# Kernel optimization log

Measured on AMD Instinct MI355X. Metric: run time of the kernel, lower is better.

Reference implementation:

```python
import jax, jax.numpy as jnp
import numpy as np

B, T, I, H, L, O = 2048, 512, 1, 64, 2, 1


def _lstm_layer(x, Wih, Whh, b):
    """Single LSTM layer, batch_first x: [B, T, in] -> [B, T, H].
    PyTorch gate order: i, f, g, o. b = b_ih + b_hh (folded)."""
    Bn = x.shape[0]
    Hn = Whh.shape[1]
    # Precompute input contribution for all timesteps (hoisted out of scan)
    xg = jnp.einsum('bti,gi->btg', x, Wih) + b  # [B, T, 4H]

    def step(carry, xg_t):
        h, c = carry
        g = xg_t + h @ Whh.T  # [B, 4H]
        i, f, gg, o = jnp.split(g, 4, axis=-1)
        i = jax.nn.sigmoid(i)
        f = jax.nn.sigmoid(f)
        gg = jnp.tanh(gg)
        o = jax.nn.sigmoid(o)
        c = f * c + i * gg
        h = o * jnp.tanh(c)
        return (h, c), h

    h0 = jnp.zeros((Bn, Hn), x.dtype)
    c0 = jnp.zeros((Bn, Hn), x.dtype)
    (_, _), hs = jax.lax.scan(step, (h0, c0), jnp.swapaxes(xg, 0, 1))  # hs: [T, B, H]
    return jnp.swapaxes(hs, 0, 1)


def setup_inputs() -> dict:
    key = jax.random.key(0)
    ks = jax.random.split(key, 11)
    s = 1.0 / np.sqrt(H)  # torch default uniform bound
    u = lambda k, shp: jax.random.uniform(k, shp, jnp.float32, -s, s)
    return {
        'x': jax.random.normal(ks[0], (B, T, I), jnp.float32),
        'Wih0': u(ks[1], (4 * H, I)),
        'Whh0': u(ks[2], (4 * H, H)),
        'bih0': u(ks[3], (4 * H,)),
        'bhh0': u(ks[4], (4 * H,)),
        'Wih1': u(ks[5], (4 * H, H)),
        'Whh1': u(ks[6], (4 * H, H)),
        'bih1': u(ks[7], (4 * H,)),
        'bhh1': u(ks[8], (4 * H,)),
        'fcW': u(ks[9], (O, H)),
        'fcb': u(ks[10], (O,)),
    }


def reference(x, Wih0, Whh0, bih0, bhh0, Wih1, Whh1, bih1, bhh1, fcW, fcb):
    h1 = _lstm_layer(x, Wih0, Whh0, bih0 + bhh0)   # [B, T, H]
    h2 = _lstm_layer(h1, Wih1, Whh1, bih1 + bhh1)  # [B, T, H]
    return h2[:, -1, :] @ fcW.T + fcb               # [B, O]
```

## Files before the change

### kernel.cpp

```cpp
#include <hip/hip_runtime.h>


#define TT 512
#define HH 64
#define BT 8

typedef __attribute__((ext_vector_type(4))) int i32x4;

#define MFMAI8 __builtin_amdgcn_mfma_i32_16x16x64_i8

#define WSCALE 260096.0f
#define HSCALE 32512.0f
#define LOG2E  1.44269504f
constexpr float C_SIG = (float)(256.0 / (260096.0 * 32512.0) * 1.4426950408889634);
constexpr float C_TGH = (float)(2.0 * 256.0 / (260096.0 * 32512.0) * 1.4426950408889634);

__device__ __forceinline__ float exp2_hw(float x) {
    float r; asm("v_exp_f32 %0, %1" : "=v"(r) : "v"(x)); return r;
}
__device__ __forceinline__ float exp2n_hw(float x) {
    float r; asm("v_exp_f32 %0, -%1" : "=v"(r) : "v"(x)); return r;
}
__device__ __forceinline__ float gate4s(float p0, float p1, float p2, float p3, float& c) {
    float gi = __builtin_amdgcn_rcpf(1.f + exp2n_hw(p0));
    float gf = __builtin_amdgcn_rcpf(1.f + exp2n_hw(p1));
    float gg = 1.f - 2.f * __builtin_amdgcn_rcpf(1.f + exp2_hw(p2));
    float go = __builtin_amdgcn_rcpf(1.f + exp2n_hw(p3));
    c = fmaf(gf, c, gi * gg);
    float tc = 1.f - 2.f * __builtin_amdgcn_rcpf(1.f + exp2_hw(c * (2.f * LOG2E)));
    return go * tc;
}
__device__ __forceinline__ int dpp_ror8_i(int v) {
    return __builtin_amdgcn_update_dpp(v, v, 0x128, 0xF, 0xF, true);
}
__device__ __forceinline__ void cvtW16(const float* __restrict__ p, i32x4& hi, i32x4& lo) {
    #pragma unroll
    for (int r = 0; r < 4; ++r) {
        int hw = 0, lw = 0;
        #pragma unroll
        for (int b = 0; b < 4; ++b) {
            int wq = (int)rintf(p[4 * b + r] * WSCALE);
            int h8 = (wq + 128) >> 8;
            int l8 = wq - (h8 << 8);
            hw |= (h8 & 0xFF) << (8 * b);
            lw |= (l8 & 0xFF) << (8 * b);
        }
        hi[r] = hw; lo[r] = lw;
    }
}

__global__ __launch_bounds__(512, 2) void lstm_mfma(
    const float* __restrict__ x,
    const float* __restrict__ Wih0, const float* __restrict__ Whh0,
    const float* __restrict__ bih0, const float* __restrict__ bhh0,
    const float* __restrict__ Wih1, const float* __restrict__ Whh1,
    const float* __restrict__ bih1, const float* __restrict__ bhh1,
    const float* __restrict__ fcW, const float* __restrict__ fcb,
    float* __restrict__ out)
{
    __shared__ float xs[BT][TT + 1];
    __shared__ __align__(16) signed char aH[2][2][2][64][16];
    __shared__ float hF[BT][HH + 1];
    __shared__ float fcw_s[HH];

    const int t    = threadIdx.x;
    const int lane = t & 63;
    const int v    = t >> 6;
    const int b0   = blockIdx.x * BT;
    const int m    = lane & 15;
    const int q    = lane >> 4;
    const int ts   = m >> 3;
    const int bpk  = m & 7;
    const int j    = 4 * (2 * v + ts) + q;

    for (int i = t; i < BT * TT; i += 512)
        xs[i >> 9][i & (TT - 1)] = x[(size_t)(b0 + (i >> 9)) * TT + (i & (TT - 1))];
    {
        int* z = (int*)aH;
        for (int i = t; i < 2048; i += 512)
            z[i] = ((i >> 8) & 1) ? 0x80808080 : 0;
    }
    if (t < HH) fcw_s[t] = fcW[t];

    i32x4 A0h[2], A0l[2], I1h[2], I1l[2], H1h[2], H1l[2];
    #pragma unroll
    for (int i = 0; i < 2; ++i) {
        const int rho = (m & 3) * 64 + 4 * (2 * v + i) + (m >> 2);
        cvtW16(Whh0 + rho * HH + q * 16, A0h[i], A0l[i]);
        cvtW16(Wih1 + rho * HH + q * 16, I1h[i], I1l[i]);
        cvtW16(Whh1 + rho * HH + q * 16, H1h[i], H1l[i]);
    }

    i32x4 corrA[2], corrB[2];
    {
        i32x4 ones; ones[0] = 0x01010101; ones[1] = 0x01010101;
        ones[2] = 0x01010101; ones[3] = 0x01010101;
        i32x4 zz = {0, 0, 0, 0};
        #pragma unroll
        for (int i = 0; i < 2; ++i) {
            i32x4 Sa = MFMAI8(A0h[i], ones, zz, 0, 0, 0);
            i32x4 Sb = MFMAI8(H1h[i], ones, MFMAI8(I1h[i], ones, zz, 0, 0, 0), 0, 0, 0);
            #pragma unroll
            for (int r = 0; r < 4; ++r) {
                corrA[i][r] = Sa[r] << 7;
                corrB[i][r] = Sb[r] << 7;
            }
        }
    }

    float wxb[4], bia1[4], bia2[4];
    #pragma unroll
    for (int g = 0; g < 4; ++g) {
        const int r = g * 64 + j;
        const float sc = (g == 2) ? 2.f * LOG2E : LOG2E;
        wxb[g]  = Wih0[r] * sc;
        bia1[g] = (bih0[r] + bhh0[r]) * sc;
        bia2[g] = (bih1[r] + bhh1[r]) * sc;
    }
    const int wl = ((j >> 4) << 4) + bpk;
    const int wb = ((j & 3) << 2) | ((j >> 2) & 3);
    float c1 = 0.f, c2 = 0.f;

    __syncthreads();

    {
        i32x4 bh1 = *(const i32x4*)&aH[0][0][0][lane][0];
        i32x4 bl1 = *(const i32x4*)&aH[0][0][1][lane][0];
        i32x4 aHH[2], aMD[2];
        #pragma unroll
        for (int i = 0; i < 2; ++i) {
            i32x4 z4 = {0, 0, 0, 0};
            aHH[i] = MFMAI8(A0h[i], bh1, z4, 0, 0, 0);
            aMD[i] = MFMAI8(A0l[i], bh1, MFMAI8(A0h[i], bl1, corrA[i], 0, 0, 0), 0, 0, 0);
        }
        float xb = xs[bpk][0];
        float pre[4];
        #pragma unroll
        for (int r = 0; r < 4; ++r) {
            int Pa = (aHH[0][r] << 8) + aMD[0][r];
            int Pb = (aHH[1][r] << 8) + aMD[1][r];
            int P  = Pa + dpp_ror8_i(Pb);
            const float Cr = (r == 2) ? C_TGH : C_SIG;
            pre[r] = fmaf((float)P, Cr, fmaf(wxb[r], xb, bia1[r]));
        }
        float h1v = gate4s(pre[0], pre[1], pre[2], pre[3], c1);
        int hq = __float_as_int(fmaf(h1v, HSCALE, 12582912.f)) - 0x4B400000;
        aH[0][1][0][wl][wb] = (signed char)(hq >> 8);
        aH[0][1][1][wl][wb] = (signed char)(hq ^ 0x80);
        __syncthreads();
    }

    #pragma unroll 2
    for (int k = 1; k < TT; ++k) {
        const int p = k & 1, pn = p ^ 1;
        i32x4 bh1 = *(const i32x4*)&aH[0][p][0][lane][0];
        i32x4 bl1 = *(const i32x4*)&aH[0][p][1][lane][0];
        i32x4 bh2 = *(const i32x4*)&aH[1][p][0][lane][0];
        i32x4 bl2 = *(const i32x4*)&aH[1][p][1][lane][0];
        float xb = xs[bpk][k];

        i32x4 aHH[2], aMD[2], bHH[2], bMD[2];
        #pragma unroll
        for (int i = 0; i < 2; ++i) {
            i32x4 z4 = {0, 0, 0, 0};
            aHH[i] = MFMAI8(A0h[i], bh1, z4, 0, 0, 0);
            aMD[i] = MFMAI8(A0l[i], bh1, MFMAI8(A0h[i], bl1, corrA[i], 0, 0, 0), 0, 0, 0);
        }
        #pragma unroll
        for (int i = 0; i < 2; ++i) {
            i32x4 z4 = {0, 0, 0, 0};
            bHH[i] = MFMAI8(H1h[i], bh2, MFMAI8(I1h[i], bh1, z4, 0, 0, 0), 0, 0, 0);
            bMD[i] = MFMAI8(H1l[i], bh2,
                     MFMAI8(H1h[i], bl2,
                     MFMAI8(I1l[i], bh1,
                     MFMAI8(I1h[i], bl1, corrB[i], 0, 0, 0), 0, 0, 0), 0, 0, 0), 0, 0, 0);
        }
        __builtin_amdgcn_sched_barrier(0);

        {
            float pre[4];
            #pragma unroll
            for (int r = 0; r < 4; ++r) {
                int Pa = (aHH[0][r] << 8) + aMD[0][r];
                int Pb = (aHH[1][r] << 8) + aMD[1][r];
                int P  = Pa + dpp_ror8_i(Pb);
                const float Cr = (r == 2) ? C_TGH : C_SIG;
                pre[r] = fmaf((float)P, Cr, fmaf(wxb[r], xb, bia1[r]));
            }
            float h1v = gate4s(pre[0], pre[1], pre[2], pre[3], c1);
            int hq = __float_as_int(fmaf(h1v, HSCALE, 12582912.f)) - 0x4B400000;
            aH[0][pn][0][wl][wb] = (signed char)(hq >> 8);
            aH[0][pn][1][wl][wb] = (signed char)(hq ^ 0x80);
        }
        __builtin_amdgcn_sched_barrier(0);

        {
            float pre[4];
            #pragma unroll
            for (int r = 0; r < 4; ++r) {
                int Pc = (bHH[0][r] << 8) + bMD[0][r];
                int Pd = (bHH[1][r] << 8) + bMD[1][r];
                int P  = Pc + dpp_ror8_i(Pd);
                const float Cr = (r == 2) ? C_TGH : C_SIG;
                pre[r] = fmaf((float)P, Cr, bia2[r]);
            }
            float h2v = gate4s(pre[0], pre[1], pre[2], pre[3], c2);
            int hq = __float_as_int(fmaf(h2v, HSCALE, 12582912.f)) - 0x4B400000;
            aH[1][pn][0][wl][wb] = (signed char)(hq >> 8);
            aH[1][pn][1][wl][wb] = (signed char)(hq ^ 0x80);
        }
        __syncthreads();
    }

    {
        i32x4 bh1 = *(const i32x4*)&aH[0][0][0][lane][0];
        i32x4 bl1 = *(const i32x4*)&aH[0][0][1][lane][0];
        i32x4 bh2 = *(const i32x4*)&aH[1][0][0][lane][0];
        i32x4 bl2 = *(const i32x4*)&aH[1][0][1][lane][0];
        i32x4 bHH[2], bMD[2];
        #pragma unroll
        for (int i = 0; i < 2; ++i) {
            i32x4 z4 = {0, 0, 0, 0};
            bHH[i] = MFMAI8(H1h[i], bh2, MFMAI8(I1h[i], bh1, z4, 0, 0, 0), 0, 0, 0);
            bMD[i] = MFMAI8(H1l[i], bh2,
                     MFMAI8(H1h[i], bl2,
                     MFMAI8(I1l[i], bh1,
                     MFMAI8(I1h[i], bl1, corrB[i], 0, 0, 0), 0, 0, 0), 0, 0, 0), 0, 0, 0);
        }
        float pre[4];
        #pragma unroll
        for (int r = 0; r < 4; ++r) {
            int Pc = (bHH[0][r] << 8) + bMD[0][r];
            int Pd = (bHH[1][r] << 8) + bMD[1][r];
            int P  = Pc + dpp_ror8_i(Pd);
            const float Cr = (r == 2) ? C_TGH : C_SIG;
            pre[r] = fmaf((float)P, Cr, bia2[r]);
        }
        float h2v = gate4s(pre[0], pre[1], pre[2], pre[3], c2);
        hF[bpk][j] = h2v;
    }
    __syncthreads();

    if (t < BT) {
        float s = fcb[0];
        #pragma unroll 8
        for (int jj = 0; jj < HH; ++jj)
            s = fmaf(hF[t][jj], fcw_s[jj], s);
        out[b0 + t] = s;
    }
}

extern "C" void kernel_launch(void* const* d_in, const int* in_sizes, int n_in,
                              void* d_out, int out_size, void* d_ws, size_t ws_size,
                              hipStream_t stream) {
    const float* x    = (const float*)d_in[0];
    const float* Wih0 = (const float*)d_in[1];
    const float* Whh0 = (const float*)d_in[2];
    const float* bih0 = (const float*)d_in[3];
    const float* bhh0 = (const float*)d_in[4];
    const float* Wih1 = (const float*)d_in[5];
    const float* Whh1 = (const float*)d_in[6];
    const float* bih1 = (const float*)d_in[7];
    const float* bhh1 = (const float*)d_in[8];
    const float* fcW  = (const float*)d_in[9];
    const float* fcb  = (const float*)d_in[10];
    float* out = (float*)d_out;

    lstm_mfma<<<dim3(2048 / BT), dim3(512), 0, stream>>>(
        x, Wih0, Whh0, bih0, bhh0, Wih1, Whh1, bih1, bhh1, fcW, fcb, out);
}
```

Baseline: 419.3 us.

## Split LSTM layers across separate wavefronts and merge gate reciprocals

Blocks grow from 512 to 1024 threads. The first 8 wavefronts compute layer 1 and the last 8 compute layer 2, so each wave holds only its own layer's weights, and layer-1 waves get raised priority with s_setprio. The gate math is rewritten to fold the i, f, g sigmoid/tanh reciprocals into one reciprocal, and o with tanh(c) into another, which cuts transcendental-unit work. The cost is more waves per block for every barrier and possible occupancy limits. The merged-denominator form can also lose precision or overflow, which the code guards only on the tanh input.

New measurement: 426.3 us. No clear change (+1.7%).

```diff
diff --git a/kernel.cpp b/kernel.cpp
--- a/kernel.cpp
+++ b/kernel.cpp
@@ -21,14 +21,20 @@
 __device__ __forceinline__ float exp2n_hw(float x) {
     float r; asm("v_exp_f32 %0, -%1" : "=v"(r) : "v"(x)); return r;
 }
-__device__ __forceinline__ float gate4s(float p0, float p1, float p2, float p3, float& c) {
-    float gi = __builtin_amdgcn_rcpf(1.f + exp2n_hw(p0));
-    float gf = __builtin_amdgcn_rcpf(1.f + exp2n_hw(p1));
-    float gg = 1.f - 2.f * __builtin_amdgcn_rcpf(1.f + exp2_hw(p2));
-    float go = __builtin_amdgcn_rcpf(1.f + exp2n_hw(p3));
-    c = fmaf(gf, c, gi * gg);
-    float tc = 1.f - 2.f * __builtin_amdgcn_rcpf(1.f + exp2_hw(c * (2.f * LOG2E)));
-    return go * tc;
+__device__ __forceinline__ float gate4f(float p0, float p1, float p2, float p3, float& c) {
+    float ia = exp2n_hw(p0);
+    float fb = exp2n_hw(p1);
+    float gb = exp2_hw(p2);
+    float ob = exp2n_hw(p3);
+    float A = 1.f + ia, B = 1.f + gb, F = 1.f + fb;
+    float t1  = A * B;
+    float den = t1 * F;
+    float num = fmaf(c, t1, (B - 2.f) * F);
+    c = num * __builtin_amdgcn_rcpf(den);
+    float e2 = exp2_hw(fminf(c * (2.f * LOG2E), 126.f));
+    float C  = 1.f + e2;
+    float r2 = __builtin_amdgcn_rcpf((1.f + ob) * C);
+    return (C - 2.f) * r2;
 }
 __device__ __forceinline__ int dpp_ror8_i(int v) {
     return __builtin_amdgcn_update_dpp(v, v, 0x128, 0xF, 0xF, true);
@@ -49,7 +55,7 @@
     }
 }
 
-__global__ __launch_bounds__(512, 2) void lstm_mfma(
+__global__ __launch_bounds__(1024) void lstm_mfma(
     const float* __restrict__ x,
     const float* __restrict__ Wih0, const float* __restrict__ Whh0,
     const float* __restrict__ bih0, const float* __restrict__ bhh0,
@@ -65,179 +71,177 @@
 
     const int t    = threadIdx.x;
     const int lane = t & 63;
-    const int v    = t >> 6;
+    const int w    = t >> 6;
+    const bool isL1 = (w < 8);
+    const int wv   = w & 7;
     const int b0   = blockIdx.x * BT;
     const int m    = lane & 15;
     const int q    = lane >> 4;
     const int ts   = m >> 3;
     const int bpk  = m & 7;
-    const int j    = 4 * (2 * v + ts) + q;
-
-    for (int i = t; i < BT * TT; i += 512)
+    const int j    = 8 * wv + 4 * ts + q;
+
+    for (int i = t; i < BT * TT; i += 1024)
         xs[i >> 9][i & (TT - 1)] = x[(size_t)(b0 + (i >> 9)) * TT + (i & (TT - 1))];
     {
         int* z = (int*)aH;
-        for (int i = t; i < 2048; i += 512)
+        for (int i = t; i < 2048; i += 1024)
             z[i] = ((i >> 8) & 1) ? 0x80808080 : 0;
     }
     if (t < HH) fcw_s[t] = fcW[t];
 
-    i32x4 A0h[2], A0l[2], I1h[2], I1l[2], H1h[2], H1l[2];
-    #pragma unroll
-    for (int i = 0; i < 2; ++i) {
-        const int rho = (m & 3) * 64 + 4 * (2 * v + i) + (m >> 2);
-        cvtW16(Whh0 + rho * HH + q * 16, A0h[i], A0l[i]);
-        cvtW16(Wih1 + rho * HH + q * 16, I1h[i], I1l[i]);
-        cvtW16(Whh1 + rho * HH + q * 16, H1h[i], H1l[i]);
-    }
-
-    i32x4 corrA[2], corrB[2];
+    i32x4 Wh[2][2], Wl[2][2];
+    i32x4 corr[2];
     {
         i32x4 ones; ones[0] = 0x01010101; ones[1] = 0x01010101;
         ones[2] = 0x01010101; ones[3] = 0x01010101;
         i32x4 zz = {0, 0, 0, 0};
         #pragma unroll
         for (int i = 0; i < 2; ++i) {
-            i32x4 Sa = MFMAI8(A0h[i], ones, zz, 0, 0, 0);
-            i32x4 Sb = MFMAI8(H1h[i], ones, MFMAI8(I1h[i], ones, zz, 0, 0, 0), 0, 0, 0);
-            #pragma unroll
-            for (int r = 0; r < 4; ++r) {
-                corrA[i][r] = Sa[r] << 7;
-                corrB[i][r] = Sb[r] << 7;
-            }
-        }
-    }
-
-    float wxb[4], bia1[4], bia2[4];
+            const int rho = (m & 3) * 64 + 4 * (2 * wv + i) + (m >> 2);
+            if (isL1) {
+                cvtW16(Whh0 + rho * HH + q * 16, Wh[i][0], Wl[i][0]);
+                i32x4 S = MFMAI8(Wh[i][0], ones, zz, 0, 0, 0);
+                #pragma unroll
+                for (int r = 0; r < 4; ++r) corr[i][r] = S[r] << 7;
+            } else {
+                cvtW16(Wih1 + rho * HH + q * 16, Wh[i][0], Wl[i][0]);
+                cvtW16(Whh1 + rho * HH + q * 16, Wh[i][1], Wl[i][1]);
+                i32x4 S = MFMAI8(Wh[i][1], ones, MFMAI8(Wh[i][0], ones, zz, 0, 0, 0), 0, 0, 0);
+                #pragma unroll
+                for (int r = 0; r < 4; ++r) corr[i][r] = S[r] << 7;
+            }
+        }
+    }
+
+    float wxb[4], bia[4];
     #pragma unroll
     for (int g = 0; g < 4; ++g) {
         const int r = g * 64 + j;
         const float sc = (g == 2) ? 2.f * LOG2E : LOG2E;
-        wxb[g]  = Wih0[r] * sc;
-        bia1[g] = (bih0[r] + bhh0[r]) * sc;
-        bia2[g] = (bih1[r] + bhh1[r]) * sc;
+        if (isL1) { wxb[g] = Wih0[r] * sc; bia[g] = (bih0[r] + bhh0[r]) * sc; }
+        else      { wxb[g] = 0.f;          bia[g] = (bih1[r] + bhh1[r]) * sc; }
     }
     const int wl = ((j >> 4) << 4) + bpk;
     const int wb = ((j & 3) << 2) | ((j >> 2) & 3);
-    float c1 = 0.f, c2 = 0.f;
+    float c = 0.f;
+
+    if (isL1) __builtin_amdgcn_s_setprio(1);
 
     __syncthreads();
 
-    {
+    if (isL1) {
         i32x4 bh1 = *(const i32x4*)&aH[0][0][0][lane][0];
         i32x4 bl1 = *(const i32x4*)&aH[0][0][1][lane][0];
-        i32x4 aHH[2], aMD[2];
+        i32x4 z4 = {0, 0, 0, 0};
+        i32x4 HHa[2], MDa[2];
         #pragma unroll
         for (int i = 0; i < 2; ++i) {
-            i32x4 z4 = {0, 0, 0, 0};
-            aHH[i] = MFMAI8(A0h[i], bh1, z4, 0, 0, 0);
-            aMD[i] = MFMAI8(A0l[i], bh1, MFMAI8(A0h[i], bl1, corrA[i], 0, 0, 0), 0, 0, 0);
+            HHa[i] = MFMAI8(Wh[i][0], bh1, z4, 0, 0, 0);
+            MDa[i] = MFMAI8(Wl[i][0], bh1, MFMAI8(Wh[i][0], bl1, corr[i], 0, 0, 0), 0, 0, 0);
         }
         float xb = xs[bpk][0];
         float pre[4];
         #pragma unroll
         for (int r = 0; r < 4; ++r) {
-            int Pa = (aHH[0][r] << 8) + aMD[0][r];
-            int Pb = (aHH[1][r] << 8) + aMD[1][r];
+            int Pa = (HHa[0][r] << 8) + MDa[0][r];
+            int Pb = (HHa[1][r] << 8) + MDa[1][r];
             int P  = Pa + dpp_ror8_i(Pb);
             const float Cr = (r == 2) ? C_TGH : C_SIG;
-            pre[r] = fmaf((float)P, Cr, fmaf(wxb[r], xb, bia1[r]));
-        }
-        float h1v = gate4s(pre[0], pre[1], pre[2], pre[3], c1);
-        int hq = __float_as_int(fmaf(h1v, HSCALE, 12582912.f)) - 0x4B400000;
+            pre[r] = fmaf((float)P, Cr, fmaf(wxb[r], xb, bia[r]));
+        }
+        float hv = gate4f(pre[0], pre[1], pre[2], pre[3], c);
+        int hq = __float_as_int(fmaf(hv, HSCALE, 12582912.f)) - 0x4B400000;
         aH[0][1][0][wl][wb] = (signed char)(hq >> 8);
         aH[0][1][1][wl][wb] = (signed char)(hq ^ 0x80);
-        __syncthreads();
-    }
+    }
+    __syncthreads();
 
     #pragma unroll 2
     for (int k = 1; k < TT; ++k) {
         const int p = k & 1, pn = p ^ 1;
-        i32x4 bh1 = *(const i32x4*)&aH[0][p][0][lane][0];
-        i32x4 bl1 = *(const i32x4*)&aH[0][p][1][lane][0];
-        i32x4 bh2 = *(const i32x4*)&aH[1][p][0][lane][0];
-        i32x4 bl2 = *(const i32x4*)&aH[1][p][1][lane][0];
-        float xb = xs[bpk][k];
-
-        i32x4 aHH[2], aMD[2], bHH[2], bMD[2];
-        #pragma unroll
-        for (int i = 0; i < 2; ++i) {
+        if (isL1) {
+            i32x4 bh1 = *(const i32x4*)&aH[0][p][0][lane][0];
+            i32x4 bl1 = *(const i32x4*)&aH[0][p][1][lane][0];
             i32x4 z4 = {0, 0, 0, 0};
-            aHH[i] = MFMAI8(A0h[i], bh1, z4, 0, 0, 0);
-            aMD[i] = MFMAI8(A0l[i], bh1, MFMAI8(A0h[i], bl1, corrA[i], 0, 0, 0), 0, 0, 0);
-        }
-        #pragma unroll
-        for (int i = 0; i < 2; ++i) {
-            i32x4 z4 = {0, 0, 0, 0};
-            bHH[i] = MFMAI8(H1h[i], bh2, MFMAI8(I1h[i], bh1, z4, 0, 0, 0), 0, 0, 0);
-            bMD[i] = MFMAI8(H1l[i], bh2,
-                     MFMAI8(H1h[i], bl2,
-                     MFMAI8(I1l[i], bh1,
-                     MFMAI8(I1h[i], bl1, corrB[i], 0, 0, 0), 0, 0, 0), 0, 0, 0), 0, 0, 0);
-        }
-        __builtin_amdgcn_sched_barrier(0);
-
-        {
+            i32x4 HHa[2], MDa[2];
+            #pragma unroll
+            for (int i = 0; i < 2; ++i) {
+                HHa[i] = MFMAI8(Wh[i][0], bh1, z4, 0, 0, 0);
+                MDa[i] = MFMAI8(Wl[i][0], bh1, MFMAI8(Wh[i][0], bl1, corr[i], 0, 0, 0), 0, 0, 0);
+            }
+            float xb = xs[bpk][k];
             float pre[4];
             #pragma unroll
             for (int r = 0; r < 4; ++r) {
-                int Pa = (aHH[0][r] << 8) + aMD[0][r];
-                int Pb = (aHH[1][r] << 8) + aMD[1][r];
+                int Pa = (HHa[0][r] << 8) + MDa[0][r];
+                int Pb = (HHa[1][r] << 8) + MDa[1][r];
                 int P  = Pa + dpp_ror8_i(Pb);
                 const float Cr = (r == 2) ? C_TGH : C_SIG;
-                pre[r] = fmaf((float)P, Cr, fmaf(wxb[r], xb, bia1[r]));
-            }
-            float h1v = gate4s(pre[0], pre[1], pre[2], pre[3], c1);
-            int hq = __float_as_int(fmaf(h1v, HSCALE, 12582912.f)) - 0x4B400000;
+                pre[r] = fmaf((float)P, Cr, fmaf(wxb[r], xb, bia[r]));
+            }
+            float hv = gate4f(pre[0], pre[1], pre[2], pre[3], c);
+            int hq = __float_as_int(fmaf(hv, HSCALE, 12582912.f)) - 0x4B400000;
             aH[0][pn][0][wl][wb] = (signed char)(hq >> 8);
             aH[0][pn][1][wl][wb] = (signed char)(hq ^ 0x80);
-        }
-        __builtin_amdgcn_sched_barrier(0);
-
-        {
+        } else {
+            i32x4 bh1 = *(const i32x4*)&aH[0][p][0][lane][0];
+            i32x4 bl1 = *(const i32x4*)&aH[0][p][1][lane][0];
+            i32x4 bh2 = *(const i32x4*)&aH[1][p][0][lane][0];
+            i32x4 bl2 = *(const i32x4*)&aH[1][p][1][lane][0];
+            i32x4 z4 = {0, 0, 0, 0};
+            i32x4 HHb[2], MDb[2];
+            #pragma unroll
+            for (int i = 0; i < 2; ++i) {
+                HHb[i] = MFMAI8(Wh[i][1], bh2, MFMAI8(Wh[i][0], bh1, z4, 0, 0, 0), 0, 0, 0);
+                MDb[i] = MFMAI8(Wl[i][1], bh2,
+                         MFMAI8(Wh[i][1], bl2,
+                         MFMAI8(Wl[i][0], bh1,
+                         MFMAI8(Wh[i][0], bl1, corr[i], 0, 0, 0), 0, 0, 0), 0, 0, 0), 0, 0, 0);
+            }
             float pre[4];
             #pragma unroll
             for (int r = 0; r < 4; ++r) {
-                int Pc = (bHH[0][r] << 8) + bMD[0][r];
-                int Pd = (bHH[1][r] << 8) + bMD[1][r];
-                int P  = Pc + dpp_ror8_i(Pd);
+                int Pa = (HHb[0][r] << 8) + MDb[0][r];
+                int Pb = (HHb[1][r] << 8) + MDb[1][r];
+                int P  = Pa + dpp_ror8_i(Pb);
                 const float Cr = (r == 2) ? C_TGH : C_SIG;
-                pre[r] = fmaf((float)P, Cr, bia2[r]);
-            }
-            float h2v = gate4s(pre[0], pre[1], pre[2], pre[3], c2);
-            int hq = __float_as_int(fmaf(h2v, HSCALE, 12582912.f)) - 0x4B400000;
+                pre[r] = fmaf((float)P, Cr, bia[r]);
+            }
+            float hv = gate4f(pre[0], pre[1], pre[2], pre[3], c);
+            int hq = __float_as_int(fmaf(hv, HSCALE, 12582912.f)) - 0x4B400000;
             aH[1][pn][0][wl][wb] = (signed char)(hq >> 8);
             aH[1][pn][1][wl][wb] = (signed char)(hq ^ 0x80);
         }
         __syncthreads();
     }
 
-    {
+    if (!isL1) {
         i32x4 bh1 = *(const i32x4*)&aH[0][0][0][lane][0];
         i32x4 bl1 = *(const i32x4*)&aH[0][0][1][lane][0];
         i32x4 bh2 = *(const i32x4*)&aH[1][0][0][lane][0];
         i32x4 bl2 = *(const i32x4*)&aH[1][0][1][lane][0];
-        i32x4 bHH[2], bMD[2];
+        i32x4 z4 = {0, 0, 0, 0};
+        i32x4 HHb[2], MDb[2];
         #pragma unroll
         for (int i = 0; i < 2; ++i) {
-            i32x4 z4 = {0, 0, 0, 0};
-            bHH[i] = MFMAI8(H1h[i], bh2, MFMAI8(I1h[i], bh1, z4, 0, 0, 0), 0, 0, 0);
-            bMD[i] = MFMAI8(H1l[i], bh2,
-                     MFMAI8(H1h[i], bl2,
-                     MFMAI8(I1l[i], bh1,
-                     MFMAI8(I1h[i], bl1, corrB[i], 0, 0, 0), 0, 0, 0), 0, 0, 0), 0, 0, 0);
+            HHb[i] = MFMAI8(Wh[i][1], bh2, MFMAI8(Wh[i][0], bh1, z4, 0, 0, 0), 0, 0, 0);
+            MDb[i] = MFMAI8(Wl[i][1], bh2,
+                     MFMAI8(Wh[i][1], bl2,
+                     MFMAI8(Wl[i][0], bh1,
+                     MFMAI8(Wh[i][0], bl1, corr[i], 0, 0, 0), 0, 0, 0), 0, 0, 0), 0, 0, 0);
         }
         float pre[4];
         #pragma unroll
         for (int r = 0; r < 4; ++r) {
-            int Pc = (bHH[0][r] << 8) + bMD[0][r];
-            int Pd = (bHH[1][r] << 8) + bMD[1][r];
-            int P  = Pc + dpp_ror8_i(Pd);
+            int Pa = (HHb[0][r] << 8) + MDb[0][r];
+            int Pb = (HHb[1][r] << 8) + MDb[1][r];
+            int P  = Pa + dpp_ror8_i(Pb);
             const float Cr = (r == 2) ? C_TGH : C_SIG;
-            pre[r] = fmaf((float)P, Cr, bia2[r]);
-        }
-        float h2v = gate4s(pre[0], pre[1], pre[2], pre[3], c2);
-        hF[bpk][j] = h2v;
+            pre[r] = fmaf((float)P, Cr, bia[r]);
+        }
+        float hv = gate4f(pre[0], pre[1], pre[2], pre[3], c);
+        hF[bpk][j] = hv;
     }
     __syncthreads();
 
@@ -266,6 +270,6 @@
     const float* fcb  = (const float*)d_in[10];
     float* out = (float*)d_out;
 
-    lstm_mfma<<<dim3(2048 / BT), dim3(512), 0, stream>>>(
+    lstm_mfma<<<dim3(2048 / BT), dim3(1024), 0, stream>>>(
         x, Wih0, Whh0, bih0, bhh0, Wih1, Whh1, bih1, bhh1, fcW, fcb, out);
 }
```

## Fuse LSTM gate reciprocals, split layer-2 MFMA chains, drop occupancy hint

Applied to the files above, without the earlier changes.

Rewrites the gate math so the cell update and output each need only one reciprocal, combining the sigmoid/tanh denominators algebraically and clamping the tanh exponent. Splits the layer-2 middle-term MFMA accumulation into two independent chains with separate correction terms to shorten the dependency chain. Drops the sched_barrier between the two layer epilogues, removes the min-blocks hint from launch_bounds, and skips the bias subtraction in the quantised store since the low bytes are unaffected. This trades extra registers and some numerical-range risk from the combined denominators for fewer transcendental ops and more instruction-level parallelism on the serial timestep path.

Result: slower. 458.1 us (+9.3%).

```diff
diff --git a/kernel.cpp b/kernel.cpp
--- a/kernel.cpp
+++ b/kernel.cpp
@@ -21,14 +21,20 @@
 __device__ __forceinline__ float exp2n_hw(float x) {
     float r; asm("v_exp_f32 %0, -%1" : "=v"(r) : "v"(x)); return r;
 }
-__device__ __forceinline__ float gate4s(float p0, float p1, float p2, float p3, float& c) {
-    float gi = __builtin_amdgcn_rcpf(1.f + exp2n_hw(p0));
-    float gf = __builtin_amdgcn_rcpf(1.f + exp2n_hw(p1));
-    float gg = 1.f - 2.f * __builtin_amdgcn_rcpf(1.f + exp2_hw(p2));
-    float go = __builtin_amdgcn_rcpf(1.f + exp2n_hw(p3));
-    c = fmaf(gf, c, gi * gg);
-    float tc = 1.f - 2.f * __builtin_amdgcn_rcpf(1.f + exp2_hw(c * (2.f * LOG2E)));
-    return go * tc;
+__device__ __forceinline__ float gate4f(float p0, float p1, float p2, float p3, float& c) {
+    float ia = exp2n_hw(p0);
+    float fb = exp2n_hw(p1);
+    float gb = exp2_hw(p2);
+    float ob = exp2n_hw(p3);
+    float A = 1.f + ia, B = 1.f + gb, F = 1.f + fb;
+    float t1  = A * B;
+    float den = t1 * F;
+    float num = fmaf(c, t1, (B - 2.f) * F);
+    c = num * __builtin_amdgcn_rcpf(den);
+    float e2 = exp2_hw(fminf(c * (2.f * LOG2E), 126.f));
+    float C  = 1.f + e2;
+    float r2 = __builtin_amdgcn_rcpf((1.f + ob) * C);
+    return (C - 2.f) * r2;
 }
 __device__ __forceinline__ int dpp_ror8_i(int v) {
     return __builtin_amdgcn_update_dpp(v, v, 0x128, 0xF, 0xF, true);
@@ -49,7 +55,7 @@
     }
 }
 
-__global__ __launch_bounds__(512, 2) void lstm_mfma(
+__global__ __launch_bounds__(512) void lstm_mfma(
     const float* __restrict__ x,
     const float* __restrict__ Wih0, const float* __restrict__ Whh0,
     const float* __restrict__ bih0, const float* __restrict__ bhh0,
@@ -91,7 +97,7 @@
         cvtW16(Whh1 + rho * HH + q * 16, H1h[i], H1l[i]);
     }
 
-    i32x4 corrA[2], corrB[2];
+    i32x4 corrA[2], corrBI[2], corrBH[2];
     {
         i32x4 ones; ones[0] = 0x01010101; ones[1] = 0x01010101;
         ones[2] = 0x01010101; ones[3] = 0x01010101;
@@ -99,11 +105,13 @@
         #pragma unroll
         for (int i = 0; i < 2; ++i) {
             i32x4 Sa = MFMAI8(A0h[i], ones, zz, 0, 0, 0);
-            i32x4 Sb = MFMAI8(H1h[i], ones, MFMAI8(I1h[i], ones, zz, 0, 0, 0), 0, 0, 0);
+            i32x4 Si = MFMAI8(I1h[i], ones, zz, 0, 0, 0);
+            i32x4 Sh = MFMAI8(H1h[i], ones, zz, 0, 0, 0);
             #pragma unroll
             for (int r = 0; r < 4; ++r) {
-                corrA[i][r] = Sa[r] << 7;
-                corrB[i][r] = Sb[r] << 7;
+                corrA[i][r]  = Sa[r] << 7;
+                corrBI[i][r] = Si[r] << 7;
+                corrBH[i][r] = Sh[r] << 7;
             }
         }
     }
@@ -143,10 +151,10 @@
             const float Cr = (r == 2) ? C_TGH : C_SIG;
             pre[r] = fmaf((float)P, Cr, fmaf(wxb[r], xb, bia1[r]));
         }
-        float h1v = gate4s(pre[0], pre[1], pre[2], pre[3], c1);
-        int hq = __float_as_int(fmaf(h1v, HSCALE, 12582912.f)) - 0x4B400000;
-        aH[0][1][0][wl][wb] = (signed char)(hq >> 8);
-        aH[0][1][1][wl][wb] = (signed char)(hq ^ 0x80);
+        float h1v = gate4f(pre[0], pre[1], pre[2], pre[3], c1);
+        int u = __float_as_int(fmaf(h1v, HSCALE, 12582912.f));
+        aH[0][1][0][wl][wb] = (signed char)(u >> 8);
+        aH[0][1][1][wl][wb] = (signed char)(u ^ 0x80);
         __syncthreads();
     }
 
@@ -159,7 +167,7 @@
         i32x4 bl2 = *(const i32x4*)&aH[1][p][1][lane][0];
         float xb = xs[bpk][k];
 
-        i32x4 aHH[2], aMD[2], bHH[2], bMD[2];
+        i32x4 aHH[2], aMD[2], bHH[2], bMD1[2], bMD2[2];
         #pragma unroll
         for (int i = 0; i < 2; ++i) {
             i32x4 z4 = {0, 0, 0, 0};
@@ -169,11 +177,9 @@
         #pragma unroll
         for (int i = 0; i < 2; ++i) {
             i32x4 z4 = {0, 0, 0, 0};
-            bHH[i] = MFMAI8(H1h[i], bh2, MFMAI8(I1h[i], bh1, z4, 0, 0, 0), 0, 0, 0);
-            bMD[i] = MFMAI8(H1l[i], bh2,
-                     MFMAI8(H1h[i], bl2,
-                     MFMAI8(I1l[i], bh1,
-                     MFMAI8(I1h[i], bl1, corrB[i], 0, 0, 0), 0, 0, 0), 0, 0, 0), 0, 0, 0);
+            bHH[i]  = MFMAI8(H1h[i], bh2, MFMAI8(I1h[i], bh1, z4, 0, 0, 0), 0, 0, 0);
+            bMD1[i] = MFMAI8(I1l[i], bh1, MFMAI8(I1h[i], bl1, corrBI[i], 0, 0, 0), 0, 0, 0);
+            bMD2[i] = MFMAI8(H1l[i], bh2, MFMAI8(H1h[i], bl2, corrBH[i], 0, 0, 0), 0, 0, 0);
         }
         __builtin_amdgcn_sched_barrier(0);
 
@@ -187,27 +193,25 @@
                 const float Cr = (r == 2) ? C_TGH : C_SIG;
                 pre[r] = fmaf((float)P, Cr, fmaf(wxb[r], xb, bia1[r]));
             }
-            float h1v = gate4s(pre[0], pre[1], pre[2], pre[3], c1);
-            int hq = __float_as_int(fmaf(h1v, HSCALE, 12582912.f)) - 0x4B400000;
-            aH[0][pn][0][wl][wb] = (signed char)(hq >> 8);
-            aH[0][pn][1][wl][wb] = (signed char)(hq ^ 0x80);
-        }
-        __builtin_amdgcn_sched_barrier(0);
-
+            float h1v = gate4f(pre[0], pre[1], pre[2], pre[3], c1);
+            int u = __float_as_int(fmaf(h1v, HSCALE, 12582912.f));
+            aH[0][pn][0][wl][wb] = (signed char)(u >> 8);
+            aH[0][pn][1][wl][wb] = (signed char)(u ^ 0x80);
+        }
         {
             float pre[4];
             #pragma unroll
             for (int r = 0; r < 4; ++r) {
-                int Pc = (bHH[0][r] << 8) + bMD[0][r];
-                int Pd = (bHH[1][r] << 8) + bMD[1][r];
+                int Pc = (bHH[0][r] << 8) + bMD1[0][r] + bMD2[0][r];
+                int Pd = (bHH[1][r] << 8) + bMD1[1][r] + bMD2[1][r];
                 int P  = Pc + dpp_ror8_i(Pd);
                 const float Cr = (r == 2) ? C_TGH : C_SIG;
                 pre[r] = fmaf((float)P, Cr, bia2[r]);
             }
-            float h2v = gate4s(pre[0], pre[1], pre[2], pre[3], c2);
-            int hq = __float_as_int(fmaf(h2v, HSCALE, 12582912.f)) - 0x4B400000;
-            aH[1][pn][0][wl][wb] = (signed char)(hq >> 8);
-            aH[1][pn][1][wl][wb] = (signed char)(hq ^ 0x80);
+            float h2v = gate4f(pre[0], pre[1], pre[2], pre[3], c2);
+            int u = __float_as_int(fmaf(h2v, HSCALE, 12582912.f));
+            aH[1][pn][0][wl][wb] = (signed char)(u >> 8);
+            aH[1][pn][1][wl][wb] = (signed char)(u ^ 0x80);
         }
         __syncthreads();
     }
@@ -217,26 +221,24 @@
         i32x4 bl1 = *(const i32x4*)&aH[0][0][1][lane][0];
         i32x4 bh2 = *(const i32x4*)&aH[1][0][0][lane][0];
         i32x4 bl2 = *(const i32x4*)&aH[1][0][1][lane][0];
-        i32x4 bHH[2], bMD[2];
-        #pragma unroll
-        for (int i = 0; i < 2; ++i) {
-            i32x4 z4 = {0, 0, 0, 0};
-            bHH[i] = MFMAI8(H1h[i], bh2, MFMAI8(I1h[i], bh1, z4, 0, 0, 0), 0, 0, 0);
-            bMD[i] = MFMAI8(H1l[i], bh2,
-                     MFMAI8(H1h[i], bl2,
-                     MFMAI8(I1l[i], bh1,
-                     MFMAI8(I1h[i], bl1, corrB[i], 0, 0, 0), 0, 0, 0), 0, 0, 0), 0, 0, 0);
+        i32x4 bHH[2], bMD1[2], bMD2[2];
+        #pragma unroll
+        for (int i = 0; i < 2; ++i) {
+            i32x4 z4 = {0, 0, 0, 0};
+            bHH[i]  = MFMAI8(H1h[i], bh2, MFMAI8(I1h[i], bh1, z4, 0, 0, 0), 0, 0, 0);
+            bMD1[i] = MFMAI8(I1l[i], bh1, MFMAI8(I1h[i], bl1, corrBI[i], 0, 0, 0), 0, 0, 0);
+            bMD2[i] = MFMAI8(H1l[i], bh2, MFMAI8(H1h[i], bl2, corrBH[i], 0, 0, 0), 0, 0, 0);
         }
         float pre[4];
         #pragma unroll
         for (int r = 0; r < 4; ++r) {
-            int Pc = (bHH[0][r] << 8) + bMD[0][r];
-            int Pd = (bHH[1][r] << 8) + bMD[1][r];
+            int Pc = (bHH[0][r] << 8) + bMD1[0][r] + bMD2[0][r];
+            int Pd = (bHH[1][r] << 8) + bMD1[1][r] + bMD2[1][r];
             int P  = Pc + dpp_ror8_i(Pd);
             const float Cr = (r == 2) ? C_TGH : C_SIG;
             pre[r] = fmaf((float)P, Cr, bia2[r]);
         }
-        float h2v = gate4s(pre[0], pre[1], pre[2], pre[3], c2);
+        float h2v = gate4f(pre[0], pre[1], pre[2], pre[3], c2);
         hF[bpk][j] = h2v;
     }
     __syncthreads();
```
